# Performance work log

Hardware: AMD Instinct MI355X
Metric: run time of the kernel (lower is better)

## Reference

```python
import jax, jax.numpy as jnp
import numpy as np

V, D, NH, HD, FF, NL, NLOOPS = 1056, 320, 5, 64, 864, 6, 8
CAP, EPS, THETA = 0.8, 1e-6, 10000.0
B, S = 8, 2048


def rmsnorm(x, w):
    return w * (x * jax.lax.rsqrt(jnp.mean(x * x, axis=-1, keepdims=True) + EPS))


def rotate_half(x):
    x1, x2 = jnp.split(x, 2, axis=-1)
    return jnp.concatenate([-x2, x1], axis=-1)


def rope_tables(seq_len):
    freqs = 1.0 / (THETA ** (jnp.arange(0, HD, 2, dtype=jnp.float32) / HD))  # [HD/2]
    t = jnp.arange(seq_len, dtype=jnp.float32)
    f = jnp.outer(t, freqs)                      # [S, HD/2]
    f = jnp.concatenate([f, f], axis=-1)         # [S, HD]
    return jnp.cos(f), jnp.sin(f)


def setup_inputs() -> dict:
    key = jax.random.key(0)
    ks = jax.random.split(key, 12)
    std = 0.02
    inp = {
        "input_ids": jax.random.randint(ks[0], (B, S), 0, V),
        "iteration": 0,
        "embedding": jax.random.normal(ks[1], (V, D), jnp.float32),
        "iter_emb": jax.random.normal(ks[2], (NLOOPS, D), jnp.float32),
        "attn_norm_w": jnp.ones((NL, D), jnp.float32),
        "Wqkv": jax.random.normal(ks[3], (NL, 3 * D, D), jnp.float32) * std,
        "wo_w": jax.random.normal(ks[4], (NL, D, D), jnp.float32) * std,
        "router_w": jax.random.normal(ks[5], (NL, D), jnp.float32) * std,
        "mlp_norm_w": jnp.ones((NL, D), jnp.float32),
        "gate_w": jax.random.normal(ks[6], (NL, FF, D), jnp.float32) * std,
        "up_w": jax.random.normal(ks[7], (NL, FF, D), jnp.float32) * std,
        "down_w": jax.random.normal(ks[8], (NL, D, FF), jnp.float32) * std,
        "final_norm_w": jnp.ones((D,), jnp.float32),
    }
    return inp


def reference(input_ids, iteration, embedding, iter_emb, attn_norm_w, Wqkv, wo_w,
              router_w, mlp_norm_w, gate_w, up_w, down_w, final_norm_w):
    batch, seq = input_ids.shape
    k = max(1, int(seq * CAP))
    cos, sin = rope_tables(seq)                 # [S, HD]
    cos4 = cos[None, :, None, :]                # [1,S,1,HD]
    sin4 = sin[None, :, None, :]

    x = embedding[input_ids]                    # [B,S,D]
    if iteration < NLOOPS:
        x = x + iter_emb[iteration][None, None, :]

    causal = jnp.tril(jnp.ones((seq, seq), dtype=bool))
    bidx = jnp.arange(batch)[:, None]           # [B,1]

    for l in range(NL):
        # --- attention block ---
        h = rmsnorm(x, attn_norm_w[l])
        qkv = (h @ Wqkv[l].T).reshape(batch, seq, 3, NH, HD)
        q, kk, v = qkv[:, :, 0], qkv[:, :, 1], qkv[:, :, 2]   # [B,S,H,HD]
        q = q * cos4 + rotate_half(q) * sin4
        kk = kk * cos4 + rotate_half(kk) * sin4
        q, kk, v = (t.transpose(0, 2, 1, 3) for t in (q, kk, v))  # [B,H,S,HD]
        scores = jnp.einsum("bhqd,bhkd->bhqk", q, kk) / np.sqrt(HD)
        scores = jnp.where(causal, scores, -jnp.inf)
        attn = jax.nn.softmax(scores, axis=-1)
        out = jnp.einsum("bhqk,bhkd->bhqd", attn, v)
        out = out.transpose(0, 2, 1, 3).reshape(batch, seq, D)
        x = x + out @ wo_w[l].T

        # --- MoD router + SwiGLU MLP on selected tokens ---
        probs = jax.nn.sigmoid(x @ router_w[l])            # [B,S]
        topk_probs, topk_idx = jax.lax.top_k(probs, k)     # [B,K]
        sel = jnp.take_along_axis(x, topk_idx[:, :, None], axis=1)  # [B,K,D]
        hs = rmsnorm(sel, mlp_norm_w[l])
        gate = jax.nn.silu(hs @ gate_w[l].T) * (hs @ up_w[l].T)
        mlp = (gate @ down_w[l].T) * topk_probs[:, :, None]         # [B,K,D]
        x = x.at[bidx, topk_idx].add(mlp)                  # unique idx: add == scatter-set+residual

    return rmsnorm(x, final_norm_w)
```

## Files before the change

### kernel.cpp

```cpp
#include <hip/hip_runtime.h>
#include <hip/hip_bf16.h>
#include <math.h>

#define VSZ 1056
#define DD 320
#define NH 5
#define HD 64
#define FF 864
#define NL 6
#define NLOOPS 8
#define BB 8
#define SL 2048
#define KK 1638
#define EPSF 1e-6f

typedef _Float16 f16x8 __attribute__((ext_vector_type(8)));
typedef _Float16 f16x4 __attribute__((ext_vector_type(4)));
typedef float floatx16 __attribute__((ext_vector_type(16)));

__device__ inline void gll16(const void* g, void* l) {
    __builtin_amdgcn_global_load_lds((const __attribute__((address_space(1))) void*)g,
                                     (__attribute__((address_space(3))) void*)l, 16, 0, 0);
}

__global__ __launch_bounds__(256) void cast5_kernel(
        const float* __restrict__ s1, const float* __restrict__ s2,
        const float* __restrict__ s3, const float* __restrict__ s4,
        const float* __restrict__ s5,
        _Float16* __restrict__ d1, _Float16* __restrict__ d2,
        _Float16* __restrict__ d3, _Float16* __restrict__ d4,
        _Float16* __restrict__ d5,
        int n1, int n2, int n3, int n4, int n5) {
    int i = blockIdx.x * 256 + threadIdx.x;
    const float* s; _Float16* d; int l = i;
    if (l < n1) { s = s1; d = d1; }
    else { l -= n1; if (l < n2) { s = s2; d = d2; }
    else { l -= n2; if (l < n3) { s = s3; d = d3; }
    else { l -= n3; if (l < n4) { s = s4; d = d4; }
    else { l -= n4; if (l >= n5) return; s = s5; d = d5; } } } }
    float4 v = ((const float4*)s)[l];
    f16x4 o = { (_Float16)v.x, (_Float16)v.y, (_Float16)v.z, (_Float16)v.w };
    *(f16x4*)(d + (size_t)l * 4) = o;
}

__global__ __launch_bounds__(256) void rope_init_kernel(float2* __restrict__ tab) {
    int i = blockIdx.x * 256 + threadIdx.x;
    int s = i >> 5, j = i & 31;
    float freq = exp2f(-(float)j * 0.4152410118609203f);
    float ang = (float)s * freq;
    tab[i] = make_float2(cosf(ang), sinf(ang));
}

__global__ __launch_bounds__(256) void embed_kernel(const int* __restrict__ ids,
        const int* __restrict__ iter, const float* __restrict__ emb,
        const float* __restrict__ iter_emb, float* __restrict__ x) {
    int i = blockIdx.x * 256 + threadIdx.x;
    int d = i % DD, bs = i / DD;
    float v = emb[(size_t)ids[bs] * DD + d];
    int it = iter[0];
    if (it < NLOOPS) v += iter_emb[it * DD + d];
    x[i] = v;
}

template<typename OT>
__global__ __launch_bounds__(256) void rmsnorm_kernel(const float* __restrict__ x,
        const float* __restrict__ w, OT* __restrict__ out, int nrows) {
    int row = blockIdx.x * 4 + (threadIdx.x >> 6);
    int lane = threadIdx.x & 63;
    if (row >= nrows) return;
    const float* xr = x + (size_t)row * DD;
    float v[5]; float ss = 0.f;
#pragma unroll
    for (int i = 0; i < 5; ++i) { v[i] = xr[lane + i * 64]; ss += v[i] * v[i]; }
#pragma unroll
    for (int o = 32; o > 0; o >>= 1) ss += __shfl_xor(ss, o);
    float r = rsqrtf(ss * (1.f / DD) + EPSF);
    OT* orow = out + (size_t)row * DD;
#pragma unroll
    for (int i = 0; i < 5; ++i) orow[lane + i * 64] = (OT)(w[lane + i * 64] * v[i] * r);
}

__global__ __launch_bounds__(256) void gather_rmsnorm_kernel(const float* __restrict__ x,
        const int* __restrict__ tkidx, const float* __restrict__ w,
        _Float16* __restrict__ out, int nrows) {
    int row = blockIdx.x * 4 + (threadIdx.x >> 6);
    int lane = threadIdx.x & 63;
    if (row >= nrows) return;
    int b = row / KK;
    int t = tkidx[row];
    const float* xr = x + ((size_t)b * SL + t) * DD;
    float v[5]; float ss = 0.f;
#pragma unroll
    for (int i = 0; i < 5; ++i) { v[i] = xr[lane + i * 64]; ss += v[i] * v[i]; }
#pragma unroll
    for (int o = 32; o > 0; o >>= 1) ss += __shfl_xor(ss, o);
    float r = rsqrtf(ss * (1.f / DD) + EPSF);
    _Float16* orow = out + (size_t)row * DD;
#pragma unroll
    for (int i = 0; i < 5; ++i) orow[lane + i * 64] = (_Float16)(w[lane + i * 64] * v[i] * r);
}

__global__ __launch_bounds__(256) void router_kernel(const float* __restrict__ x,
        const float* __restrict__ rw, float* __restrict__ probs, int nrows) {
    int row = blockIdx.x * 4 + (threadIdx.x >> 6);
    int lane = threadIdx.x & 63;
    if (row >= nrows) return;
    const float* xr = x + (size_t)row * DD;
    float ss = 0.f;
#pragma unroll
    for (int i = 0; i < 5; ++i) ss += xr[lane + i * 64] * rw[lane + i * 64];
#pragma unroll
    for (int o = 32; o > 0; o >>= 1) ss += __shfl_xor(ss, o);
    if (lane == 0) probs[row] = 1.f / (1.f + __expf(-ss));
}

__global__ __launch_bounds__(1024) void topk_kernel(const float* __restrict__ probs,
        int* __restrict__ tkidx, float* __restrict__ tkprob) {
    __shared__ int hist[256];
    __shared__ int scn[256];
    __shared__ int outc;
    __shared__ int s_digit, s_rem;
    int b = blockIdx.x, tid = threadIdx.x;
    unsigned long long k0, k1;
    {
        unsigned int f0 = __float_as_uint(probs[b * SL + tid]);
        unsigned int f1 = __float_as_uint(probs[b * SL + tid + 1024]);
        k0 = ((unsigned long long)f0 << 32) | (unsigned int)(2047 - tid);
        k1 = ((unsigned long long)f1 << 32) | (unsigned int)(2047 - (tid + 1024));
    }
    if (tid == 0) outc = 0;
    unsigned long long prefix = 0, pmask = 0;
    int target = KK;
    for (int shift = 56; shift >= 0; shift -= 8) {
        if (tid < 256) hist[tid] = 0;
        __syncthreads();
        bool a0 = (k0 & pmask) == prefix;
        bool a1 = (k1 & pmask) == prefix;
        int d0 = (int)((k0 >> shift) & 255);
        int d1 = (int)((k1 >> shift) & 255);
        if (a0) atomicAdd(&hist[d0], 1);
        if (a1) atomicAdd(&hist[d1], 1);
        __syncthreads();
        if (tid < 64) {
            int h0 = hist[tid * 4], h1 = hist[tid * 4 + 1];
            int h2 = hist[tid * 4 + 2], h3 = hist[tid * 4 + 3];
            int s3 = h3, s2 = h2 + s3, s1 = h1 + s2, s0 = h0 + s1;
            int s = s0;
#pragma unroll
            for (int off = 1; off < 64; off <<= 1) {
                int v = __shfl_down(s, off);
                if (tid + off >= 64) v = 0;
                s += v;
            }
            int A = s - s0;
            scn[tid * 4]     = s0 + A;
            scn[tid * 4 + 1] = s1 + A;
            scn[tid * 4 + 2] = s2 + A;
            scn[tid * 4 + 3] = s3 + A;
        }
        __syncthreads();
        if (tid < 256 && hist[tid] > 0) {
            int S = scn[tid];
            int Sgt = S - hist[tid];
            if (Sgt < target && target <= S) { s_digit = tid; s_rem = target - Sgt; }
        }
        __syncthreads();
        int dsel = s_digit, rem = s_rem;
        bool full = (rem == hist[dsel]);
        if (a0 && (d0 > dsel || (full && d0 == dsel))) {
            int s = atomicAdd(&outc, 1);
            tkidx[b * KK + s] = 2047 - (int)(k0 & 0xffffffffu);
            tkprob[b * KK + s] = __uint_as_float((unsigned int)(k0 >> 32));
        }
        if (a1 && (d1 > dsel || (full && d1 == dsel))) {
            int s = atomicAdd(&outc, 1);
            tkidx[b * KK + s] = 2047 - (int)(k1 & 0xffffffffu);
            tkprob[b * KK + s] = __uint_as_float((unsigned int)(k1 >> 32));
        }
        if (full) break;
        target = rem;
        prefix |= ((unsigned long long)dsel) << shift;
        pmask  |= ((unsigned long long)255) << shift;
        __syncthreads();
    }
}

__global__ __launch_bounds__(256, 2) void attn_mfma(const _Float16* __restrict__ Qh,
        const _Float16* __restrict__ Kt, const _Float16* __restrict__ Vt,
        _Float16* __restrict__ attn_out) {
    __shared__ float red[4][32][32];
    __shared__ float msh[4][32];
    __shared__ float lsh[4][32];
    int tid = threadIdx.x;
    int w = tid >> 6;
    int lane = tid & 63;
    int l31 = lane & 31, h5 = lane >> 5;
    int g = blockIdx.x;
    int j = g >> 3;
    int bh = (g & 7) + 8 * (j >> 6);
    int qt = 63 - (j & 63);
    int b = bh / NH, h = bh % NH;
    int nt = (qt >> 1) + 1;
    int qw = qt * 32;
    int myq = qw + l31;

    f16x8 qf[4];
    const _Float16* qrow = Qh + ((size_t)bh * SL + myq) * 64;
#pragma unroll
    for (int kd = 0; kd < 4; ++kd) qf[kd] = *(const f16x8*)(qrow + kd * 16 + h5 * 8);

    const _Float16* Kb = Kt + (size_t)bh * 32 * 4096;
    const _Float16* Vb = Vt + (size_t)bh * 32 * 4096;

    floatx16 O0, O1;
#pragma unroll
    for (int r = 0; r < 16; ++r) { O0[r] = 0.f; O1[r] = 0.f; }
    float m = -INFINITY, l = 0.f;

    for (int t = w; t < nt; t += 4) {
        const _Float16* kb = Kb + (size_t)t * 4096;
        const _Float16* vb = Vb + (size_t)t * 4096;
        f16x8 a0[4], a1[4], v0[4], v1[4];
#pragma unroll
        for (int kd = 0; kd < 4; ++kd) {
            int off = (kd * 2 + h5) * 512 + l31 * 8;
            a0[kd] = *(const f16x8*)(kb + off);
            a1[kd] = *(const f16x8*)(kb + off + 256);
        }
#pragma unroll
        for (int kc = 0; kc < 4; ++kc) {
            int off = (kc * 2 + h5) * 512 + l31 * 8;
            v0[kc] = *(const f16x8*)(vb + off);
            v1[kc] = *(const f16x8*)(vb + off + 256);
        }
        floatx16 S0, S1;
#pragma unroll
        for (int r = 0; r < 16; ++r) { S0[r] = 0.f; S1[r] = 0.f; }
#pragma unroll
        for (int kd = 0; kd < 4; ++kd) {
            S0 = __builtin_amdgcn_mfma_f32_32x32x16_f16(a0[kd], qf[kd], S0, 0, 0, 0);
            S1 = __builtin_amdgcn_mfma_f32_32x32x16_f16(a1[kd], qf[kd], S1, 0, 0, 0);
        }
        int t0 = t * 64;
        if (t0 + 63 > qw) {
#pragma unroll
            for (int r = 0; r < 16; ++r) {
                int key = t0 + (r & 3) + 8 * (r >> 2) + 4 * h5;
                if (key > myq) S0[r] = -INFINITY;
                if (key + 32 > myq) S1[r] = -INFINITY;
            }
        }
        float tmax = S0[0];
#pragma unroll
        for (int r = 1; r < 16; ++r) tmax = fmaxf(tmax, S0[r]);
#pragma unroll
        for (int r = 0; r < 16; ++r) tmax = fmaxf(tmax, S1[r]);
        tmax = fmaxf(tmax, __shfl_xor(tmax, 32));
        if (__any(tmax > m + 8.f)) {
            float mnew = fmaxf(m, tmax);
            float alpha = exp2f(m - mnew);
            l *= alpha; O0 *= alpha; O1 *= alpha; m = mnew;
        }
        float P0[16], P1[16]; float psum = 0.f;
#pragma unroll
        for (int r = 0; r < 16; ++r) { P0[r] = exp2f(S0[r] - m); psum += P0[r]; }
#pragma unroll
        for (int r = 0; r < 16; ++r) { P1[r] = exp2f(S1[r] - m); psum += P1[r]; }
        psum += __shfl_xor(psum, 32);
        l += psum;
#pragma unroll
        for (int sub = 0; sub < 2; ++sub) {
            const float* P = sub ? P1 : P0;
#pragma unroll
            for (int kc = 0; kc < 2; ++kc) {
                auto q01 = __builtin_amdgcn_cvt_pkrtz(P[kc * 8 + 0], P[kc * 8 + 1]);
                auto q23 = __builtin_amdgcn_cvt_pkrtz(P[kc * 8 + 2], P[kc * 8 + 3]);
                auto q45 = __builtin_amdgcn_cvt_pkrtz(P[kc * 8 + 4], P[kc * 8 + 5]);
                auto q67 = __builtin_amdgcn_cvt_pkrtz(P[kc * 8 + 6], P[kc * 8 + 7]);
                f16x8 pf;
                pf[0] = (_Float16)q01[0]; pf[1] = (_Float16)q01[1];
                pf[2] = (_Float16)q23[0]; pf[3] = (_Float16)q23[1];
                pf[4] = (_Float16)q45[0]; pf[5] = (_Float16)q45[1];
                pf[6] = (_Float16)q67[0]; pf[7] = (_Float16)q67[1];
                int ksg = sub * 2 + kc;
                O0 = __builtin_amdgcn_mfma_f32_32x32x16_f16(v0[ksg], pf, O0, 0, 0, 0);
                O1 = __builtin_amdgcn_mfma_f32_32x32x16_f16(v1[ksg], pf, O1, 0, 0, 0);
            }
        }
    }
    if (h5 == 0) msh[w][l31] = m;
    __syncthreads();
    float M = fmaxf(fmaxf(msh[0][l31], msh[1][l31]), fmaxf(msh[2][l31], msh[3][l31]));
    float wgt = exp2f(m - M);
    if (h5 == 0) lsh[w][l31] = l * wgt;
#pragma unroll
    for (int r = 0; r < 16; ++r) {
        int d = (r & 3) + 8 * (r >> 2) + 4 * h5;
        red[w][d][l31] = O0[r] * wgt;
    }
    __syncthreads();
    float lsum = lsh[0][l31] + lsh[1][l31] + lsh[2][l31] + lsh[3][l31];
    float linv = 1.f / lsum;
    if (w < 2) {
        f16x8 ov;
#pragma unroll
        for (int k = 0; k < 8; ++k) {
            int d = w * 16 + h5 * 8 + k;
            ov[k] = (_Float16)((red[0][d][l31] + red[1][d][l31] +
                                red[2][d][l31] + red[3][d][l31]) * linv);
        }
        *(f16x8*)(attn_out + ((size_t)(b * SL + myq)) * DD + h * 64 + w * 16 + h5 * 8) = ov;
    }
    __syncthreads();
#pragma unroll
    for (int r = 0; r < 16; ++r) {
        int d = (r & 3) + 8 * (r >> 2) + 4 * h5;
        red[w][d][l31] = O1[r] * wgt;
    }
    __syncthreads();
    if (w >= 2) {
        f16x8 ov;
#pragma unroll
        for (int k = 0; k < 8; ++k) {
            int d = (w - 2) * 16 + h5 * 8 + k;
            ov[k] = (_Float16)((red[0][d][l31] + red[1][d][l31] +
                                red[2][d][l31] + red[3][d][l31]) * linv);
        }
        *(f16x8*)(attn_out + ((size_t)(b * SL + myq)) * DD + h * 64 + 32 + (w - 2) * 16 + h5 * 8) = ov;
    }
}

__global__ __launch_bounds__(256) void gemm_qkv(const _Float16* __restrict__ A,
        const _Float16* __restrict__ W, const float2* __restrict__ ropet,
        _Float16* __restrict__ Qh, _Float16* __restrict__ Kt, _Float16* __restrict__ Vt,
        int M, int N, int K, int nn_tiles) {
    __shared__ __attribute__((aligned(16))) _Float16 As[2][2048];
    __shared__ __attribute__((aligned(16))) _Float16 Ws[2][4096];
    int tid = threadIdx.x;
    int lane = tid & 63;
    int wave = tid >> 6;
    int l31 = lane & 31, h5 = lane >> 5;
    int nwg = gridDim.x;
    int q = nwg >> 3, r = nwg & 7;
    int xcd = blockIdx.x & 7, idx = blockIdx.x >> 3;
    int wgid = (xcd < r ? xcd * (q + 1) : r * (q + 1) + (xcd - r) * q) + idx;
    int mt = wgid / nn_tiles;
    int nt = wgid - mt * nn_tiles;
    int m0 = mt * 64, n0 = nt * 128;
    int wm = (wave & 1) * 32, wn2 = (wave >> 1) * 64;

    int srA = tid & 63, skA = tid >> 6;
    int srW = tid & 127, skW = tid >> 7;
    int arow = m0 + srA; if (arow >= M) arow = M - 1;
    int wrow = n0 + srW; if (wrow >= N) wrow = N - 1;
    const _Float16* Ag = A + (size_t)arow * K + skA * 8;
    const _Float16* Wg = W + (size_t)wrow * K + skW * 8;
    _Float16* AsD = As[0] + (size_t)(tid & ~63) * 8;
    _Float16* WsD = Ws[0] + (size_t)(tid & ~63) * 8;

    floatx16 acc0, acc1;
#pragma unroll
    for (int i = 0; i < 16; ++i) { acc0[i] = 0.f; acc1[i] = 0.f; }

    gll16(Ag, AsD);
    gll16(Wg, WsD);
    gll16(Wg + 16, WsD + 2048);
    __syncthreads();

    int nk = K >> 5;
    for (int t = 0; t < nk; ++t) {
        int buf = t & 1;
        if (t + 1 < nk) {
            int k0 = (t + 1) * 32;
            int bo = buf ^ 1;
            gll16(Ag + k0, AsD + bo * 2048);
            gll16(Wg + k0, WsD + bo * 4096);
            gll16(Wg + k0 + 16, WsD + bo * 4096 + 2048);
        }
        const _Float16* Asb = As[buf];
        const _Float16* Wsb = Ws[buf];
#pragma unroll
        for (int ks = 0; ks < 2; ++ks) {
            int kc = ks * 2 + h5;
            f16x8 a  = *(const f16x8*)(Asb + kc * 512 + (wm + l31) * 8);
            f16x8 b0 = *(const f16x8*)(Wsb + kc * 1024 + (wn2 + l31) * 8);
            f16x8 b1 = *(const f16x8*)(Wsb + kc * 1024 + (wn2 + 32 + l31) * 8);
            acc0 = __builtin_amdgcn_mfma_f32_32x32x16_f16(a, b0, acc0, 0, 0, 0);
            acc1 = __builtin_amdgcn_mfma_f32_32x32x16_f16(a, b1, acc1, 0, 0, 0);
        }
        __syncthreads();
    }

    int nb0 = n0 + wn2;
    if (nb0 >= N) return;
    int comp = nb0 / DD;
    int hh = (nb0 % DD) / 64;
    const float QS = 0.125f * 1.44269504088896341f;
    if (comp == 2) {
#pragma unroll
        for (int r2 = 0; r2 < 16; ++r2) {
            int mm = m0 + wm + (r2 & 3) + 8 * (r2 >> 2) + 4 * h5;
            int b = mm >> 11, s = mm & 2047;
            int key = s & 63;
            int kc8 = ((key >> 4) << 1) | ((key >> 2) & 1);
            int jj = (key & 3) | (((key >> 3) & 1) << 2);
            size_t vbase = (((size_t)(b * NH + hh) * 32 + (s >> 6)) * 8 + kc8) * 512 + jj;
            Vt[vbase + (size_t)l31 * 8] = (_Float16)acc0[r2];
            Vt[vbase + (size_t)(l31 + 32) * 8] = (_Float16)acc1[r2];
        }
    } else {
#pragma unroll
        for (int r2 = 0; r2 < 16; ++r2) {
            int mm = m0 + wm + (r2 & 3) + 8 * (r2 >> 2) + 4 * h5;
            int b = mm >> 11, s = mm & 2047;
            float2 cs = ropet[(size_t)s * 32 + l31];
            float lo = acc0[r2], hi = acc1[r2];
            float ro0 = lo * cs.x - hi * cs.y;
            float ro1 = hi * cs.x + lo * cs.y;
            if (comp == 0) {
                _Float16* qp = Qh + ((size_t)(b * NH + hh) * SL + s) * 64;
                qp[l31] = (_Float16)(ro0 * QS);
                qp[l31 + 32] = (_Float16)(ro1 * QS);
            } else {
                size_t kb2 = (((size_t)(b * NH + hh) * 32 + (s >> 6)) * 8) * 512 + (s & 63) * 8;
                Kt[kb2 + (size_t)(l31 >> 3) * 512 + (l31 & 7)] = (_Float16)ro0;
                Kt[kb2 + (size_t)((l31 + 32) >> 3) * 512 + (l31 & 7)] = (_Float16)ro1;
            }
        }
    }
}

template<int MODE>
__global__ __launch_bounds__(256) void gemm_mfma(const _Float16* __restrict__ A,
        const _Float16* __restrict__ W, _Float16* __restrict__ Ch, float* __restrict__ X,
        int M, int N, int K, int nn_tiles, const int* __restrict__ sidx, const float* __restrict__ sprob) {
    __shared__ __attribute__((aligned(16))) _Float16 As[2][4096];
    __shared__ __attribute__((aligned(16))) _Float16 Ws[2][4096];
    int tid = threadIdx.x;
    int lane = tid & 63;
    int wave = tid >> 6;
    int l31 = lane & 31, h5 = lane >> 5;
    int nwg = gridDim.x;
    int q = nwg >> 3, r = nwg & 7;
    int xcd = blockIdx.x & 7, idx = blockIdx.x >> 3;
    int wgid = (xcd < r ? xcd * (q + 1) : r * (q + 1) + (xcd - r) * q) + idx;
    int mt = wgid / nn_tiles;
    int nt = wgid - mt * nn_tiles;
    int m0 = mt * 64, n0 = nt * 64;
    int wm = (wave & 1) * 32, wn = (wave >> 1) * 32;

    int srow = tid & 63;
    int skc = tid >> 6;
    int arow = m0 + srow; if (arow >= M) arow = M - 1;
    int wrow = n0 + srow; if (wrow >= N) wrow = N - 1;
    const _Float16* Ag = A + (size_t)arow * K + skc * 8;
    const _Float16* Wg = W + (size_t)wrow * K + skc * 8;
    _Float16* AsD = As[0] + (size_t)(tid & ~63) * 8;
    _Float16* WsD = Ws[0] + (size_t)(tid & ~63) * 8;

    floatx16 acc;
#pragma unroll
    for (int i = 0; i < 16; ++i) acc[i] = 0.f;

    int nk32 = K >> 5;
    int nfull = nk32 >> 1;
    int tail = nk32 & 1;

    gll16(Ag, AsD);
    gll16(Wg, WsD);
    gll16(Ag + 32, AsD + 2048);
    gll16(Wg + 32, WsD + 2048);
    __syncthreads();

    for (int t = 0; t < nfull; ++t) {
        int buf = t & 1;
        int bo = (buf ^ 1) * 4096;
        if (t + 1 < nfull) {
            int k0 = (t + 1) * 64;
            gll16(Ag + k0, AsD + bo);
            gll16(Wg + k0, WsD + bo);
            gll16(Ag + k0 + 32, AsD + bo + 2048);
            gll16(Wg + k0 + 32, WsD + bo + 2048);
        } else if (tail) {
            int k0 = nfull * 64;
            gll16(Ag + k0, AsD + bo);
            gll16(Wg + k0, WsD + bo);
        }
        const _Float16* Asb = As[buf];
        const _Float16* Wsb = Ws[buf];
#pragma unroll
        for (int ks = 0; ks < 4; ++ks) {
            int kc = ks * 2 + h5;
            f16x8 a = *(const f16x8*)(Asb + kc * 512 + (wm + l31) * 8);
            f16x8 b = *(const f16x8*)(Wsb + kc * 512 + (wn + l31) * 8);
            acc = __builtin_amdgcn_mfma_f32_32x32x16_f16(a, b, acc, 0, 0, 0);
        }
        __syncthreads();
    }
    if (tail) {
        int buf = nfull & 1;
        const _Float16* Asb = As[buf];
        const _Float16* Wsb = Ws[buf];
#pragma unroll
        for (int ks = 0; ks < 2; ++ks) {
            int kc = ks * 2 + h5;
            f16x8 a = *(const f16x8*)(Asb + kc * 512 + (wm + l31) * 8);
            f16x8 b = *(const f16x8*)(Wsb + kc * 512 + (wn + l31) * 8);
            acc = __builtin_amdgcn_mfma_f32_32x32x16_f16(a, b, acc, 0, 0, 0);
        }
    }

    int nn = n0 + wn + l31;
#pragma unroll
    for (int r2 = 0; r2 < 16; ++r2) {
        int mm = m0 + wm + (r2 & 3) + 8 * (r2 >> 2) + 4 * h5;
        if (mm >= M || nn >= N) continue;
        float v = acc[r2];
        if (MODE == 1) {
            X[(size_t)mm * N + nn] += v;
        } else {
            int b = mm / KK;
            X[((size_t)(b * SL + sidx[mm])) * N + nn] += v * sprob[mm];
        }
    }
}

__global__ __launch_bounds__(256) void gemm_gateup(const _Float16* __restrict__ A,
        const _Float16* __restrict__ Wg, const _Float16* __restrict__ Wu,
        _Float16* __restrict__ Ch, int M, int N, int K, int nn_tiles) {
    __shared__ __attribute__((aligned(16))) _Float16 As[2][2048];
    __shared__ __attribute__((aligned(16))) _Float16 Wgs[2][4096];
    __shared__ __attribute__((aligned(16))) _Float16 Wus[2][4096];
    int tid = threadIdx.x;
    int lane = tid & 63;
    int wave = tid >> 6;
    int l31 = lane & 31, h5 = lane >> 5;
    int nwg = gridDim.x;
    int q = nwg >> 3, r = nwg & 7;
    int xcd = blockIdx.x & 7, idx = blockIdx.x >> 3;
    int wgid = (xcd < r ? xcd * (q + 1) : r * (q + 1) + (xcd - r) * q) + idx;
    int mt = wgid / nn_tiles;
    int nt = wgid - mt * nn_tiles;
    int m0 = mt * 64, n0 = nt * 128;
    int wm = (wave & 1) * 32, wn2 = (wave >> 1) * 64;

    int srA = tid & 63, skA = tid >> 6;
    int srW = tid & 127, skW = tid >> 7;
    int arow = m0 + srA; if (arow >= M) arow = M - 1;
    int wrow = n0 + srW; if (wrow >= N) wrow = N - 1;
    const _Float16* Ag  = A  + (size_t)arow * K + skA * 8;
    const _Float16* Wgg = Wg + (size_t)wrow * K + skW * 8;
    const _Float16* Wug = Wu + (size_t)wrow * K + skW * 8;
    _Float16* AsD  = As[0]  + (size_t)(tid & ~63) * 8;
    _Float16* WgsD = Wgs[0] + (size_t)(tid & ~63) * 8;
    _Float16* WusD = Wus[0] + (size_t)(tid & ~63) * 8;

    floatx16 ag0, ag1, au0, au1;
#pragma unroll
    for (int i = 0; i < 16; ++i) { ag0[i] = 0.f; ag1[i] = 0.f; au0[i] = 0.f; au1[i] = 0.f; }

    gll16(Ag, AsD);
    gll16(Wgg, WgsD);
    gll16(Wgg + 16, WgsD + 2048);
    gll16(Wug, WusD);
    gll16(Wug + 16, WusD + 2048);
    __syncthreads();

    int nk = K >> 5;
    for (int t = 0; t < nk; ++t) {
        int buf = t & 1;
        if (t + 1 < nk) {
            int k0 = (t + 1) * 32;
            int bo = buf ^ 1;
            gll16(Ag + k0, AsD + bo * 2048);
            gll16(Wgg + k0, WgsD + bo * 4096);
            gll16(Wgg + k0 + 16, WgsD + bo * 4096 + 2048);
            gll16(Wug + k0, WusD + bo * 4096);
            gll16(Wug + k0 + 16, WusD + bo * 4096 + 2048);
        }
        const _Float16* Asb = As[buf];
        const _Float16* Wgb = Wgs[buf];
        const _Float16* Wub = Wus[buf];
#pragma unroll
        for (int ks = 0; ks < 2; ++ks) {
            int kc = ks * 2 + h5;
            f16x8 a  = *(const f16x8*)(Asb + kc * 512 + (wm + l31) * 8);
            f16x8 g0 = *(const f16x8*)(Wgb + kc * 1024 + (wn2 + l31) * 8);
            f16x8 g1 = *(const f16x8*)(Wgb + kc * 1024 + (wn2 + 32 + l31) * 8);
            f16x8 u0 = *(const f16x8*)(Wub + kc * 1024 + (wn2 + l31) * 8);
            f16x8 u1 = *(const f16x8*)(Wub + kc * 1024 + (wn2 + 32 + l31) * 8);
            ag0 = __builtin_amdgcn_mfma_f32_32x32x16_f16(a, g0, ag0, 0, 0, 0);
            au0 = __builtin_amdgcn_mfma_f32_32x32x16_f16(a, u0, au0, 0, 0, 0);
            ag1 = __builtin_amdgcn_mfma_f32_32x32x16_f16(a, g1, ag1, 0, 0, 0);
            au1 = __builtin_amdgcn_mfma_f32_32x32x16_f16(a, u1, au1, 0, 0, 0);
        }
        __syncthreads();
    }

#pragma unroll
    for (int nj = 0; nj < 2; ++nj) {
        int nn = n0 + wn2 + nj * 32 + l31;
        if (nn >= N) continue;
        const floatx16& gA = nj ? ag1 : ag0;
        const floatx16& uA = nj ? au1 : au0;
#pragma unroll
        for (int r2 = 0; r2 < 16; ++r2) {
            int mm = m0 + wm + (r2 & 3) + 8 * (r2 >> 2) + 4 * h5;
            if (mm >= M) continue;
            float gv = gA[r2], uv = uA[r2];
            Ch[(size_t)mm * N + nn] = (_Float16)((gv / (1.f + __expf(-gv))) * uv);
        }
    }
}

extern "C" void kernel_launch(void* const* d_in, const int* in_sizes, int n_in,
                              void* d_out, int out_size, void* d_ws, size_t ws_size,
                              hipStream_t stream) {
    const int*   ids          = (const int*)d_in[0];
    const int*   iter         = (const int*)d_in[1];
    const float* emb          = (const float*)d_in[2];
    const float* iter_emb     = (const float*)d_in[3];
    const float* attn_norm_w  = (const float*)d_in[4];
    const float* Wqkv         = (const float*)d_in[5];
    const float* wo_w         = (const float*)d_in[6];
    const float* router_w     = (const float*)d_in[7];
    const float* mlp_norm_w   = (const float*)d_in[8];
    const float* gate_w       = (const float*)d_in[9];
    const float* up_w         = (const float*)d_in[10];
    const float* down_w       = (const float*)d_in[11];
    const float* final_norm_w = (const float*)d_in[12];
    float* out = (float*)d_out;

    const size_t XN   = (size_t)BB * SL * DD;
    const size_t QKVN = (size_t)BB * SL * 3 * DD;
    const size_t HN   = (size_t)BB * NH * SL * 64;
    char* ws = (char*)d_ws;
    size_t off = 0;
    float*    x        = (float*)(ws + off);    off += XN * 4;
    _Float16* h        = (_Float16*)(ws + off); off += XN * 2;
    _Float16* attn_out = (_Float16*)(ws + off); off += XN * 2;
    float*    probs    = (float*)(ws + off);    off += (size_t)BB * SL * 4;
    int*      tkidx    = (int*)(ws + off);      off += (size_t)BB * KK * 4;
    float*    tkprob   = (float*)(ws + off);    off += (size_t)BB * KK * 4;
    off = (off + 255) & ~(size_t)255;
    _Float16* qkvh     = (_Float16*)(ws + off); off += QKVN * 2;
    _Float16* Qh       = (_Float16*)(ws + off); off += HN * 2;
    _Float16* Kh       = (_Float16*)(ws + off); off += HN * 2;
    _Float16* Vh       = (_Float16*)(ws + off); off += HN * 2;
    float2*   ropet    = (float2*)(ws + off);   off += (size_t)SL * 32 * 8;
    _Float16* WqkvH    = (_Float16*)(ws + off);
    _Float16* woH   = WqkvH + (size_t)NL * 3 * DD * DD;
    _Float16* gateH = woH   + (size_t)NL * DD * DD;
    _Float16* upH   = gateH + (size_t)NL * FF * DD;
    _Float16* downH = upH   + (size_t)NL * FF * DD;
    _Float16* g1 = qkvh;

    rope_init_kernel<<<SL * 32 / 256, 256, 0, stream>>>(ropet);
    {
        int n1 = NL * 3 * DD * DD / 4, n2 = NL * DD * DD / 4;
        int n3 = NL * FF * DD / 4, n4 = NL * FF * DD / 4, n5 = NL * DD * FF / 4;
        int ntot = n1 + n2 + n3 + n4 + n5;
        cast5_kernel<<<(ntot + 255) / 256, 256, 0, stream>>>(
            Wqkv, wo_w, gate_w, up_w, down_w,
            WqkvH, woH, gateH, upH, downH, n1, n2, n3, n4, n5);
    }

    embed_kernel<<<20480, 256, 0, stream>>>(ids, iter, emb, iter_emb, x);

    const int M1 = BB * SL;
    const int M2 = BB * KK;
    const int MT1 = (M1 + 63) / 64;
    const int MT2 = (M2 + 63) / 64;
    for (int l = 0; l < NL; ++l) {
        rmsnorm_kernel<_Float16><<<4096, 256, 0, stream>>>(x, attn_norm_w + l * DD, h, M1);
        gemm_qkv<<<MT1 * 8, 256, 0, stream>>>(h, WqkvH + (size_t)l * 3 * DD * DD,
                                              ropet, Qh, Kh, Vh, M1, 3 * DD, DD, 8);
        attn_mfma<<<BB * NH * (SL / 32), 256, 0, stream>>>(Qh, Kh, Vh, attn_out);
        gemm_mfma<1><<<MT1 * 5, 256, 0, stream>>>(attn_out, woH + (size_t)l * DD * DD,
                                                  nullptr, x, M1, DD, DD, 5, nullptr, nullptr);
        router_kernel<<<4096, 256, 0, stream>>>(x, router_w + l * DD, probs, M1);
        topk_kernel<<<BB, 1024, 0, stream>>>(probs, tkidx, tkprob);
        gather_rmsnorm_kernel<<<3276, 256, 0, stream>>>(x, tkidx, mlp_norm_w + l * DD, h, M2);
        gemm_gateup<<<MT2 * 7, 256, 0, stream>>>(h, gateH + (size_t)l * FF * DD,
                                                 upH + (size_t)l * FF * DD, g1, M2, FF, DD, 7);
        gemm_mfma<2><<<MT2 * 5, 256, 0, stream>>>(g1, downH + (size_t)l * DD * FF,
                                                  nullptr, x, M2, DD, FF, 5, tkidx, tkprob);
    }
    rmsnorm_kernel<float><<<4096, 256, 0, stream>>>(x, final_norm_w, out, M1);
}
```

Before: 1.484 ms.

## Fuse router dot product into pre-attention rmsnorm and wo GEMM epilogue

Removes the standalone router kernel by using linearity: the router logit of x+attn·Wo is computed as the dot of the pre-attention x (in the rmsnorm kernel) plus per-tile partial dots from the wo GEMM epilogue. The top-k kernel sums ten partials and applies the sigmoid. This saves a full read of x per layer and one launch. In exchange it adds shuffle reductions and partial stores in the GEMM epilogue, and a different summation order can change near-tie top-k selections.

```diff
diff --git a/kernel.cpp b/kernel.cpp
--- a/kernel.cpp
+++ b/kernel.cpp
@@ -64,17 +64,23 @@
 
 template<typename OT>
 __global__ __launch_bounds__(256) void rmsnorm_kernel(const float* __restrict__ x,
-        const float* __restrict__ w, OT* __restrict__ out, int nrows) {
+        const float* __restrict__ w, const float* __restrict__ rw,
+        OT* __restrict__ out, float* __restrict__ rdot, int nrows) {
     int row = blockIdx.x * 4 + (threadIdx.x >> 6);
     int lane = threadIdx.x & 63;
     if (row >= nrows) return;
     const float* xr = x + (size_t)row * DD;
-    float v[5]; float ss = 0.f;
+    float v[5]; float ss = 0.f, rd = 0.f;
 #pragma unroll
     for (int i = 0; i < 5; ++i) { v[i] = xr[lane + i * 64]; ss += v[i] * v[i]; }
-#pragma unroll
-    for (int o = 32; o > 0; o >>= 1) ss += __shfl_xor(ss, o);
+    if (rw) {
+#pragma unroll
+        for (int i = 0; i < 5; ++i) rd += v[i] * rw[lane + i * 64];
+    }
+#pragma unroll
+    for (int o = 32; o > 0; o >>= 1) { ss += __shfl_xor(ss, o); if (rw) rd += __shfl_xor(rd, o); }
     float r = rsqrtf(ss * (1.f / DD) + EPSF);
+    if (rw && lane == 0) rdot[row] = rd;
     OT* orow = out + (size_t)row * DD;
 #pragma unroll
     for (int i = 0; i < 5; ++i) orow[lane + i * 64] = (OT)(w[lane + i * 64] * v[i] * r);
@@ -100,21 +106,8 @@
     for (int i = 0; i < 5; ++i) orow[lane + i * 64] = (_Float16)(w[lane + i * 64] * v[i] * r);
 }
 
-__global__ __launch_bounds__(256) void router_kernel(const float* __restrict__ x,
-        const float* __restrict__ rw, float* __restrict__ probs, int nrows) {
-    int row = blockIdx.x * 4 + (threadIdx.x >> 6);
-    int lane = threadIdx.x & 63;
-    if (row >= nrows) return;
-    const float* xr = x + (size_t)row * DD;
-    float ss = 0.f;
-#pragma unroll
-    for (int i = 0; i < 5; ++i) ss += xr[lane + i * 64] * rw[lane + i * 64];
-#pragma unroll
-    for (int o = 32; o > 0; o >>= 1) ss += __shfl_xor(ss, o);
-    if (lane == 0) probs[row] = 1.f / (1.f + __expf(-ss));
-}
-
-__global__ __launch_bounds__(1024) void topk_kernel(const float* __restrict__ probs,
+__global__ __launch_bounds__(1024) void topk_kernel(const float* __restrict__ rdot0,
+        const float* __restrict__ rpart,
         int* __restrict__ tkidx, float* __restrict__ tkprob) {
     __shared__ int hist[256];
     __shared__ int scn[256];
@@ -123,8 +116,17 @@
     int b = blockIdx.x, tid = threadIdx.x;
     unsigned long long k0, k1;
     {
-        unsigned int f0 = __float_as_uint(probs[b * SL + tid]);
-        unsigned int f1 = __float_as_uint(probs[b * SL + tid + 1024]);
+        int row0 = b * SL + tid, row1 = row0 + 1024;
+        float raw0 = rdot0[row0], raw1 = rdot0[row1];
+#pragma unroll
+        for (int i = 0; i < 10; ++i) {
+            raw0 += rpart[(size_t)i * (BB * SL) + row0];
+            raw1 += rpart[(size_t)i * (BB * SL) + row1];
+        }
+        float p0 = 1.f / (1.f + __expf(-raw0));
+        float p1 = 1.f / (1.f + __expf(-raw1));
+        unsigned int f0 = __float_as_uint(p0);
+        unsigned int f1 = __float_as_uint(p1);
         k0 = ((unsigned long long)f0 << 32) | (unsigned int)(2047 - tid);
         k1 = ((unsigned long long)f1 << 32) | (unsigned int)(2047 - (tid + 1024));
     }
@@ -432,8 +434,10 @@
 
 template<int MODE>
 __global__ __launch_bounds__(256) void gemm_mfma(const _Float16* __restrict__ A,
-        const _Float16* __restrict__ W, _Float16* __restrict__ Ch, float* __restrict__ X,
-        int M, int N, int K, int nn_tiles, const int* __restrict__ sidx, const float* __restrict__ sprob) {
+        const _Float16* __restrict__ W, float* __restrict__ X,
+        int M, int N, int K, int nn_tiles, const int* __restrict__ sidx,
+        const float* __restrict__ sprob, const float* __restrict__ rw,
+        float* __restrict__ rpart) {
     __shared__ __attribute__((aligned(16))) _Float16 As[2][4096];
     __shared__ __attribute__((aligned(16))) _Float16 Ws[2][4096];
     int tid = threadIdx.x;
@@ -511,6 +515,8 @@
     }
 
     int nn = n0 + wn + l31;
+    float rwv = 0.f;
+    if (MODE == 1) rwv = rw[nn];
 #pragma unroll
     for (int r2 = 0; r2 < 16; ++r2) {
         int mm = m0 + wm + (r2 & 3) + 8 * (r2 >> 2) + 4 * h5;
@@ -518,6 +524,10 @@
         float v = acc[r2];
         if (MODE == 1) {
             X[(size_t)mm * N + nn] += v;
+            float p = v * rwv;
+#pragma unroll
+            for (int off = 16; off > 0; off >>= 1) p += __shfl_xor(p, off);
+            if (l31 == 0) rpart[(size_t)(nt * 2 + (wave >> 1)) * M + mm] = p;
         } else {
             int b = mm / KK;
             X[((size_t)(b * SL + sidx[mm])) * N + nn] += v * sprob[mm];
@@ -639,7 +649,8 @@
     float*    x        = (float*)(ws + off);    off += XN * 4;
     _Float16* h        = (_Float16*)(ws + off); off += XN * 2;
     _Float16* attn_out = (_Float16*)(ws + off); off += XN * 2;
-    float*    probs    = (float*)(ws + off);    off += (size_t)BB * SL * 4;
+    float*    rdot0    = (float*)(ws + off);    off += (size_t)BB * SL * 4;
+    float*    rpart    = (float*)(ws + off);    off += (size_t)10 * BB * SL * 4;
     int*      tkidx    = (int*)(ws + off);      off += (size_t)BB * KK * 4;
     float*    tkprob   = (float*)(ws + off);    off += (size_t)BB * KK * 4;
     off = (off + 255) & ~(size_t)255;
@@ -672,19 +683,21 @@
     const int MT1 = (M1 + 63) / 64;
     const int MT2 = (M2 + 63) / 64;
     for (int l = 0; l < NL; ++l) {
-        rmsnorm_kernel<_Float16><<<4096, 256, 0, stream>>>(x, attn_norm_w + l * DD, h, M1);
+        rmsnorm_kernel<_Float16><<<4096, 256, 0, stream>>>(x, attn_norm_w + l * DD,
+                                                           router_w + l * DD, h, rdot0, M1);
         gemm_qkv<<<MT1 * 8, 256, 0, stream>>>(h, WqkvH + (size_t)l * 3 * DD * DD,
                                               ropet, Qh, Kh, Vh, M1, 3 * DD, DD, 8);
         attn_mfma<<<BB * NH * (SL / 32), 256, 0, stream>>>(Qh, Kh, Vh, attn_out);
         gemm_mfma<1><<<MT1 * 5, 256, 0, stream>>>(attn_out, woH + (size_t)l * DD * DD,
-                                                  nullptr, x, M1, DD, DD, 5, nullptr, nullptr);
-        router_kernel<<<4096, 256, 0, stream>>>(x, router_w + l * DD, probs, M1);
-        topk_kernel<<<BB, 1024, 0, stream>>>(probs, tkidx, tkprob);
+                                                  x, M1, DD, DD, 5, nullptr, nullptr,
+                                                  router_w + l * DD, rpart);
+        topk_kernel<<<BB, 1024, 0, stream>>>(rdot0, rpart, tkidx, tkprob);
         gather_rmsnorm_kernel<<<3276, 256, 0, stream>>>(x, tkidx, mlp_norm_w + l * DD, h, M2);
         gemm_gateup<<<MT2 * 7, 256, 0, stream>>>(h, gateH + (size_t)l * FF * DD,
                                                  upH + (size_t)l * FF * DD, g1, M2, FF, DD, 7);
         gemm_mfma<2><<<MT2 * 5, 256, 0, stream>>>(g1, downH + (size_t)l * DD * FF,
-                                                  nullptr, x, M2, DD, FF, 5, tkidx, tkprob);
-    }
-    rmsnorm_kernel<float><<<4096, 256, 0, stream>>>(x, final_norm_w, out, M1);
-}
+                                                  x, M2, DD, FF, 5, tkidx, tkprob,
+                                                  nullptr, nullptr);
+    }
+    rmsnorm_kernel<float><<<4096, 256, 0, stream>>>(x, final_norm_w, nullptr, out, nullptr, M1);
+}
```

Measured after the change: 1.495 ms. Within noise of the previous version (+0.7%).
